# Kernel optimization log

Hardware: AMD Instinct MI355X
Metric: run time of the kernel (lower is better)

## Reference

```python
import jax, jax.numpy as jnp
import numpy as np

B, L, P, S, O = 8192, 512, 64, 32, 200
BIG = jnp.float32(1e30)


def setup_inputs() -> dict:
    key = jax.random.key(0)
    k1, k2, k3, k4, k5 = jax.random.split(key, 5)
    x = jax.random.normal(k1, (B, L), dtype=jnp.float32)
    # nn.init.uniform_ default is U[0,1)
    prototypes = jax.random.uniform(k2, (P, L), dtype=jnp.float32)
    sub_prototypes = jax.random.uniform(k3, (P, S, L), dtype=jnp.float32)
    # per-group linear layers: weight [O,S], bias [O], stacked over P groups
    lim = 1.0 / np.sqrt(S)
    W = jax.random.uniform(k4, (P, O, S), dtype=jnp.float32, minval=-lim, maxval=lim)
    b = jax.random.uniform(k5, (P, O), dtype=jnp.float32, minval=-lim, maxval=lim)
    return {"x": x, "prototypes": prototypes, "sub_prototypes": sub_prototypes, "W": W, "b": b}


def reference(x, prototypes, sub_prototypes, W, b):
    # pairwise squared euclidean distances to top-level prototypes: [B, P]
    d_top = (jnp.sum(x * x, axis=1)[:, None]
             + jnp.sum(prototypes * prototypes, axis=1)[None, :]
             - 2.0 * x @ prototypes.T)
    min1 = jnp.mean(jnp.min(d_top, axis=1))
    min2 = jnp.mean(jnp.min(d_top, axis=0))
    idx = jnp.argmin(d_top, axis=1)  # [B] top-1 routing

    # distances of every sample to every group's sub-prototypes: [B, P, S]
    cross = jnp.einsum('bl,psl->bps', x, sub_prototypes)
    d_all = (jnp.sum(x * x, axis=1)[:, None, None]
             + jnp.sum(sub_prototypes * sub_prototypes, axis=2)[None, :, :]
             - 2.0 * cross)

    # gather each sample's own group's sub-distances: [B, S]
    d_sel = jnp.take_along_axis(d_all, idx[:, None, None], axis=1)[:, 0, :]

    # per-group linear expert applied to gathered rows, scattered back: [B, O]
    out = jnp.einsum('bs,bos->bo', d_sel, W[idx]) + b[idx]

    member = idx[:, None] == jnp.arange(P)[None, :]  # [B, P]
    counts = jnp.sum(member, axis=0)                 # [P]
    nonempty = counts > 0

    # sub_min1: per group, min over assigned samples per sub-proto, mean over S
    d_masked = jnp.where(member[:, :, None], d_all, BIG)
    grp_min_over_b = jnp.min(d_masked, axis=0)       # [P, S]
    per_grp_m1 = jnp.mean(grp_min_over_b, axis=1)    # [P]
    sub_min1 = jnp.sum(jnp.where(nonempty, per_grp_m1, 0.0)) / P

    # sub_min2: per group, mean over assigned samples of per-sample min over S
    per_sample_min = jnp.min(d_sel, axis=1)          # [B]
    grp_sum = jax.ops.segment_sum(per_sample_min, idx, num_segments=P)  # [P]
    per_grp_m2 = jnp.where(nonempty, grp_sum / jnp.maximum(counts, 1), 0.0)
    sub_min2 = jnp.sum(per_grp_m2) / P

    return (min1, min2, sub_min1, sub_min2, out)
```

## Files before the change

### kernel.cpp

```cpp
#include <hip/hip_runtime.h>


#define NL 512
#define NP 64
#define NS 32
#define NO 200
#define NB 8192
#define MAXCH 192

#define WS_SUM     0
#define WS_COLMIN  1
#define WS_SUBMIN  65
#define WS_GRPSUM  2113
#define WS_COUNT   2177
#define WS_PP      2241
#define WS_SP2     2305
#define WS_C2G     4353
#define WS_CBASE   4545
#define WS_CMCNT   4737
#define WS_OFFS    4929
#define WS_SS      4994
#define WS_IDX     13186
#define WS_ORDER   21378
#define WB_PB_HI   131072
#define WB_PB_LO   196608
#define WB_SPB_HI  262144
#define WB_SPB_LO  2359296

typedef __attribute__((ext_vector_type(8))) short short8v;
typedef __attribute__((ext_vector_type(4))) float f32x4;

__device__ __forceinline__ unsigned encf(float f) {
  unsigned u = __float_as_uint(f);
  return (u & 0x80000000u) ? ~u : (u | 0x80000000u);
}
__device__ __forceinline__ float decf(unsigned m) {
  return __uint_as_float((m & 0x80000000u) ? (m ^ 0x80000000u) : ~m);
}
__device__ __forceinline__ float wred(float v) {
#pragma unroll
  for (int m = 32; m >= 1; m >>= 1) v += __shfl_xor(v, m, 64);
  return v;
}
__device__ __forceinline__ float dot4(const float4& a, const float4& b) {
  return a.x * b.x + a.y * b.y + a.z * b.z + a.w * b.w;
}
__device__ __forceinline__ unsigned short f2bf(float f) {
  unsigned u = __float_as_uint(f);
  u += 0x7FFFu + ((u >> 16) & 1u);
  return (unsigned short)(u >> 16);
}
__device__ __forceinline__ float bf2f(unsigned short h) {
  return __uint_as_float(((unsigned)h) << 16);
}
__device__ __forceinline__ void cvt8(const float4& v0, const float4& v1,
                                     short8v& hi, short8v& lo, float& ss) {
  float vs[8] = {v0.x, v0.y, v0.z, v0.w, v1.x, v1.y, v1.z, v1.w};
#pragma unroll
  for (int i = 0; i < 8; ++i) {
    ss = fmaf(vs[i], vs[i], ss);
    unsigned short h = f2bf(vs[i]);
    hi[i] = (short)h;
    lo[i] = (short)f2bf(vs[i] - bf2f(h));
  }
}

__global__ __launch_bounds__(256) void hier_prep(const float* __restrict__ proto,
                                                 const float* __restrict__ subp,
                                                 float* __restrict__ ws) {
  __shared__ float part[256];
  const int bid = blockIdx.x, tid = threadIdx.x;
  unsigned short* sph = (unsigned short*)((char*)ws + WB_SPB_HI);
  unsigned short* spl = (unsigned short*)((char*)ws + WB_SPB_LO);
  unsigned short* pbh = (unsigned short*)((char*)ws + WB_PB_HI);
  unsigned short* pbl = (unsigned short*)((char*)ws + WB_PB_LO);

  if (bid < 512) {
    const int fi = bid * 256 + tid;
    const int l = fi & 63, nt = (fi >> 6) & 1, kt = (fi >> 7) & 15, g = fi >> 11;
    const int s = nt * 16 + (l & 15), k0 = kt * 32 + (l >> 4) * 8;
    const float* src = subp + ((size_t)(g * NS + s)) * NL + k0;
    float4 a = *(const float4*)src, b = *(const float4*)(src + 4);
    float vs[8] = {a.x, a.y, a.z, a.w, b.x, b.y, b.z, b.w};
#pragma unroll
    for (int i = 0; i < 8; ++i) {
      unsigned short h = f2bf(vs[i]);
      sph[(size_t)fi * 8 + i] = h;
      spl[(size_t)fi * 8 + i] = f2bf(vs[i] - bf2f(h));
    }
    return;
  }
  if (bid < 528) {
    const int pi = (bid - 512) * 256 + tid;
    const int l = pi & 63, nt = (pi >> 6) & 3, kt = pi >> 8;
    const int p = nt * 16 + (l & 15), k0 = kt * 32 + (l >> 4) * 8;
    const float* src = proto + (size_t)p * NL + k0;
    float4 a = *(const float4*)src, b = *(const float4*)(src + 4);
    float vs[8] = {a.x, a.y, a.z, a.w, b.x, b.y, b.z, b.w};
#pragma unroll
    for (int i = 0; i < 8; ++i) {
      unsigned short h = f2bf(vs[i]);
      pbh[(size_t)pi * 8 + i] = h;
      pbl[(size_t)pi * 8 + i] = f2bf(vs[i] - bf2f(h));
    }
    return;
  }
  if (bid < 560) {
    const int r = (bid - 528) * 64 + (tid >> 2), q = tid & 3;
    const float4* src = (const float4*)(subp + (size_t)r * NL) + q * 32;
    float a = 0.f;
#pragma unroll
    for (int j = 0; j < 32; ++j) a += dot4(src[j], src[j]);
    part[tid] = a;
    __syncthreads();
    if (tid < 64)
      ws[WS_SP2 + (bid - 528) * 64 + tid] =
          part[4 * tid] + part[4 * tid + 1] + part[4 * tid + 2] + part[4 * tid + 3];
    return;
  }
  if (bid == 560) {
    const int r = tid >> 2, q = tid & 3;
    const float4* src = (const float4*)(proto + (size_t)r * NL) + q * 32;
    float a = 0.f;
#pragma unroll
    for (int j = 0; j < 32; ++j) a += dot4(src[j], src[j]);
    part[tid] = a;
    __syncthreads();
    if (tid < 64)
      ws[WS_PP + tid] =
          part[4 * tid] + part[4 * tid + 1] + part[4 * tid + 2] + part[4 * tid + 3];
    return;
  }
  unsigned* wsu = (unsigned*)ws;
  if (tid == 0) ws[WS_SUM] = 0.f;
  if (tid < 64) {
    wsu[WS_COLMIN + tid] = 0xFFFFFFFFu;
    ws[WS_GRPSUM + tid] = 0.f;
    wsu[WS_COUNT + tid] = 0u;
  }
  for (int u = tid; u < NP * NS; u += 256) wsu[WS_SUBMIN + u] = 0xFFFFFFFFu;
}

__global__ __launch_bounds__(256) void hier_phase1(const float* __restrict__ x,
                                                   float* __restrict__ ws) {
  __shared__ unsigned hist_l[64];
  const int tid = threadIdx.x, lane = tid & 63, w = tid >> 6;
  const int c = lane & 15, g4 = lane >> 4;
  const int b0 = blockIdx.x * 64;
  const short8v* PBH = (const short8v*)((const char*)ws + WB_PB_HI);
  const short8v* PBL = (const short8v*)((const char*)ws + WB_PB_LO);
  if (tid < 64) hist_l[tid] = 0u;
  __syncthreads();

  const int row = b0 + w * 16 + c;
  const float* xrow = x + (size_t)row * NL + g4 * 8;
  f32x4 acc[4];
#pragma unroll
  for (int nt = 0; nt < 4; ++nt) acc[nt] = (f32x4){0.f, 0.f, 0.f, 0.f};
  float ssv = 0.f;

#pragma unroll 2
  for (int kt = 0; kt < 16; ++kt) {
    float4 v0 = *(const float4*)(xrow + kt * 32);
    float4 v1 = *(const float4*)(xrow + kt * 32 + 4);
    short8v ah, al;
    cvt8(v0, v1, ah, al, ssv);
    const short8v* BH = PBH + (size_t)(kt * 4) * 64 + lane;
    const short8v* BL = PBL + (size_t)(kt * 4) * 64 + lane;
#pragma unroll
    for (int nt = 0; nt < 4; ++nt) {
      short8v bh = BH[nt * 64];
      short8v bl = BL[nt * 64];
      acc[nt] = __builtin_amdgcn_mfma_f32_16x16x32_bf16(ah, bh, acc[nt], 0, 0, 0);
      acc[nt] = __builtin_amdgcn_mfma_f32_16x16x32_bf16(ah, bl, acc[nt], 0, 0, 0);
      acc[nt] = __builtin_amdgcn_mfma_f32_16x16x32_bf16(al, bh, acc[nt], 0, 0, 0);
    }
  }

  ssv += __shfl_xor(ssv, 16, 64);
  ssv += __shfl_xor(ssv, 32, 64);
  if (lane < 16) ws[WS_SS + b0 + w * 16 + lane] = ssv;
  float ssm[4];
#pragma unroll
  for (int r = 0; r < 4; ++r) ssm[r] = __shfl(ssv, g4 * 4 + r, 64);

  float dv[4][4];
#pragma unroll
  for (int nt = 0; nt < 4; ++nt) {
    float ppv = ws[WS_PP + nt * 16 + c];
#pragma unroll
    for (int r = 0; r < 4; ++r) dv[nt][r] = ssm[r] + ppv - 2.f * acc[nt][r];
  }
  float rmin[4];
  int rarg[4];
#pragma unroll
  for (int r = 0; r < 4; ++r) {
    rmin[r] = 1e30f; rarg[r] = 0;
#pragma unroll
    for (int nt = 0; nt < 4; ++nt)
      if (dv[nt][r] < rmin[r]) { rmin[r] = dv[nt][r]; rarg[r] = nt * 16 + c; }
  }
#pragma unroll
  for (int m = 1; m <= 8; m <<= 1) {
#pragma unroll
    for (int r = 0; r < 4; ++r) {
      float om = __shfl_xor(rmin[r], m, 64);
      int oa = __shfl_xor(rarg[r], m, 64);
      if (om < rmin[r] || (om == rmin[r] && oa < rarg[r])) { rmin[r] = om; rarg[r] = oa; }
    }
  }
#pragma unroll
  for (int nt = 0; nt < 4; ++nt) {
    float cm = fminf(fminf(dv[nt][0], dv[nt][1]), fminf(dv[nt][2], dv[nt][3]));
    cm = fminf(cm, __shfl_xor(cm, 16, 64));
    cm = fminf(cm, __shfl_xor(cm, 32, 64));
    if (lane < 16) atomicMin((unsigned*)ws + WS_COLMIN + nt * 16 + lane, encf(cm));
  }
  float rsum = 0.f;
  if (c == 0) {
#pragma unroll
    for (int r = 0; r < 4; ++r) {
      ((int*)ws)[WS_IDX + b0 + w * 16 + g4 * 4 + r] = rarg[r];
      atomicAdd(&hist_l[rarg[r]], 1u);
      rsum += rmin[r];
    }
  }
  rsum = wred(rsum);
  if (lane == 0) atomicAdd(&ws[WS_SUM], rsum);
  __syncthreads();
  if (tid < 64 && hist_l[tid]) atomicAdd((unsigned*)ws + WS_COUNT + tid, hist_l[tid]);
}

__global__ __launch_bounds__(256) void hier_scan(float* __restrict__ ws) {
  __shared__ unsigned cnt_l[64];
  __shared__ unsigned cur[64];
  const int tid = threadIdx.x;
  unsigned* wsu = (unsigned*)ws;
  for (int i = tid; i < MAXCH; i += 256) ((int*)ws)[WS_C2G + i] = -1;
  if (tid < 64) cnt_l[tid] = wsu[WS_COUNT + tid];
  __syncthreads();
  if (tid == 0) {
    unsigned run = 0;
    int nc = 0;
    for (int g = 0; g < NP; ++g) {
      wsu[WS_OFFS + g] = run;
      unsigned cc = cnt_l[g];
      for (unsigned j = 0; j * 64 < cc; ++j) {
        ((int*)ws)[WS_C2G + nc] = g;
        wsu[WS_CBASE + nc] = run + j * 64;
        unsigned mc = cc - j * 64;
        wsu[WS_CMCNT + nc] = mc < 64u ? mc : 64u;
        ++nc;
      }
      run += cc;
    }
    wsu[WS_OFFS + 64] = run;
  }
  __syncthreads();
  if (tid < 64) cur[tid] = wsu[WS_OFFS + tid];
  __syncthreads();
  const int* idx = (const int*)ws + WS_IDX;
  for (int b = tid; b < NB; b += 256) {
    int g = idx[b];
    unsigned pos = atomicAdd(&cur[g], 1u);
    wsu[WS_ORDER + pos] = (unsigned)b;
  }
}

__global__ __launch_bounds__(256) void hier_phase3(const float* __restrict__ x,
                                                   const float* __restrict__ Wm,
                                                   const float* __restrict__ bias,
                                                   float* __restrict__ out,
                                                   float* __restrict__ ws) {
  __shared__ unsigned rows_l[64];
  __shared__ float ss_l[64];
  __shared__ float sp2_l[32];
  __shared__ float dsel_l[64 * 33];
  const int tid = threadIdx.x, lane = tid & 63, w = tid >> 6;
  const int c = lane & 15, g4 = lane >> 4;
  const int ch = blockIdx.x;
  const int graw = ((const int*)ws)[WS_C2G + ch];
  if (graw < 0) return;
  const int g = graw;
  const unsigned base = ((const unsigned*)ws)[WS_CBASE + ch];
  const int mc = (int)((const unsigned*)ws)[WS_CMCNT + ch];

  if (tid < 64) {
    int m = tid < mc ? tid : mc - 1;
    rows_l[tid] = ((const unsigned*)ws)[WS_ORDER + base + m];
  }
  __syncthreads();
  if (tid < 64) ss_l[tid] = ws[WS_SS + rows_l[tid]];
  if (tid < 32) sp2_l[tid] = ws[WS_SP2 + g * NS + tid];
  __syncthreads();

  const short8v* SPH = (const short8v*)((const char*)ws + WB_SPB_HI);
  const short8v* SPL = (const short8v*)((const char*)ws + WB_SPB_LO);
  const float* xrow = x + (size_t)rows_l[w * 16 + c] * NL + g4 * 8;

  f32x4 acc[2];
  acc[0] = (f32x4){0.f, 0.f, 0.f, 0.f};
  acc[1] = (f32x4){0.f, 0.f, 0.f, 0.f};
  float ssv = 0.f;

#pragma unroll 2
  for (int kt = 0; kt < 16; ++kt) {
    float4 v0 = *(const float4*)(xrow + kt * 32);
    float4 v1 = *(const float4*)(xrow + kt * 32 + 4);
    short8v ah, al;
    cvt8(v0, v1, ah, al, ssv);
    const short8v* BH = SPH + ((size_t)(g * 16 + kt) * 2) * 64 + lane;
    const short8v* BL = SPL + ((size_t)(g * 16 + kt) * 2) * 64 + lane;
#pragma unroll
    for (int nt = 0; nt < 2; ++nt) {
      short8v bh = BH[nt * 64];
      short8v bl = BL[nt * 64];
      acc[nt] = __builtin_amdgcn_mfma_f32_16x16x32_bf16(ah, bh, acc[nt], 0, 0, 0);
      acc[nt] = __builtin_amdgcn_mfma_f32_16x16x32_bf16(ah, bl, acc[nt], 0, 0, 0);
      acc[nt] = __builtin_amdgcn_mfma_f32_16x16x32_bf16(al, bh, acc[nt], 0, 0, 0);
    }
  }

  float dv[2][4];
#pragma unroll
  for (int nt = 0; nt < 2; ++nt) {
    float s2 = sp2_l[nt * 16 + c];
#pragma unroll
    for (int r = 0; r < 4; ++r) {
      dv[nt][r] = ss_l[w * 16 + g4 * 4 + r] + s2 - 2.f * acc[nt][r];
      dsel_l[(w * 16 + g4 * 4 + r) * 33 + nt * 16 + c] = dv[nt][r];
    }
  }
#pragma unroll
  for (int nt = 0; nt < 2; ++nt) {
    float cm = fminf(fminf(dv[nt][0], dv[nt][1]), fminf(dv[nt][2], dv[nt][3]));
    cm = fminf(cm, __shfl_xor(cm, 16, 64));
    cm = fminf(cm, __shfl_xor(cm, 32, 64));
    if (lane < 16) atomicMin((unsigned*)ws + WS_SUBMIN + g * NS + nt * 16 + lane, encf(cm));
  }
  float rmin[4];
#pragma unroll
  for (int r = 0; r < 4; ++r) rmin[r] = fminf(dv[0][r], dv[1][r]);
#pragma unroll
  for (int m = 1; m <= 8; m <<= 1) {
#pragma unroll
    for (int r = 0; r < 4; ++r) rmin[r] = fminf(rmin[r], __shfl_xor(rmin[r], m, 64));
  }
  float rsum = 0.f;
  if (c == 0) {
#pragma unroll
    for (int r = 0; r < 4; ++r) {
      int sm = w * 16 + g4 * 4 + r;
      if (sm < mc) rsum += rmin[r];
    }
  }
  rsum = wred(rsum);
  if (lane == 0) atomicAdd(&ws[WS_GRPSUM + g], rsum);
  __syncthreads();

  const unsigned myrow = rows_l[lane];
  float dsr[NS];
#pragma unroll
  for (int cc = 0; cc < NS; ++cc) dsr[cc] = dsel_l[lane * 33 + cc];
  const float* wbase = Wm + (size_t)g * NO * NS;
  const float* bbase = bias + (size_t)g * NO;
  const int o0 = w * 52;
  const int no4 = (w < 3) ? 13 : 11;
  float* orow = out + (size_t)myrow * NO;
  for (int j4 = 0; j4 < no4; ++j4) {
    float rr[4];
#pragma unroll
    for (int e = 0; e < 4; ++e) {
      const int o = o0 + 4 * j4 + e;
      const float4* wv = (const float4*)(wbase + (size_t)o * NS);
      float a = bbase[o];
#pragma unroll
      for (int k = 0; k < 8; ++k) {
        float4 w4 = wv[k];
        a += dsr[4 * k + 0] * w4.x + dsr[4 * k + 1] * w4.y +
             dsr[4 * k + 2] * w4.z + dsr[4 * k + 3] * w4.w;
      }
      rr[e] = a;
    }
    float4 st = {rr[0], rr[1], rr[2], rr[3]};
    *(float4*)(orow + o0 + 4 * j4) = st;
  }
}

__global__ void hier_final(const float* __restrict__ ws, float* __restrict__ out4) {
  const int lane = threadIdx.x;
  const unsigned* colmin = (const unsigned*)ws + WS_COLMIN;
  const unsigned* submin = (const unsigned*)ws + WS_SUBMIN;
  const float* grp_sum = ws + WS_GRPSUM;
  const unsigned* counts = (const unsigned*)ws + WS_COUNT;

  float min2 = wred(decf(colmin[lane])) * (1.0f / NP);

  unsigned cnt = counts[lane];
  float s32 = 0.f;
#pragma unroll
  for (int s = 0; s < NS; s++) s32 += decf(submin[lane * NS + s]);
  float sub1 = wred((cnt > 0u) ? s32 * (1.0f / NS) : 0.f) * (1.0f / NP);
  float sub2 = wred((cnt > 0u) ? grp_sum[lane] / (float)cnt : 0.f) * (1.0f / NP);

  if (lane == 0) {
    out4[0] = ws[WS_SUM] * (1.0f / NB);
    out4[1] = min2;
    out4[2] = sub1;
    out4[3] = sub2;
  }
}

extern "C" void kernel_launch(void* const* d_in, const int* in_sizes, int n_in,
                              void* d_out, int out_size, void* d_ws, size_t ws_size,
                              hipStream_t stream) {
  const float* x = (const float*)d_in[0];
  const float* proto = (const float*)d_in[1];
  const float* subp = (const float*)d_in[2];
  const float* Wm = (const float*)d_in[3];
  const float* bias = (const float*)d_in[4];
  float* outf = (float*)d_out;
  float* ws = (float*)d_ws;

  hipLaunchKernelGGL(hier_prep, dim3(562), dim3(256), 0, stream, proto, subp, ws);
  hipLaunchKernelGGL(hier_phase1, dim3(128), dim3(256), 0, stream, x, ws);
  hipLaunchKernelGGL(hier_scan, dim3(1), dim3(256), 0, stream, ws);
  hipLaunchKernelGGL(hier_phase3, dim3(MAXCH), dim3(256), 0, stream,
                     x, Wm, bias, outf + 4, ws);
  hipLaunchKernelGGL(hier_final, dim3(1), dim3(64), 0, stream, ws, outf);
}
```

Measured before the change: 175.7 us.

## Pre-convert x to bf16 fragments, split K across waves, shrink chunks to 16 rows

x is converted once in the prep kernel into hi/lo bf16 MFMA fragment layout, and its row norms are computed there. A new reorder kernel gathers each routed chunk's fragments into a contiguous buffer. Phase1 and phase3 now split the K dimension across four waves and reduce the partial sums through shared memory. Chunks shrink from 64 to 16 rows, and MAXCH grows to 576, to raise block-level parallelism on the small grids. The expert linear layer keeps W rows in registers per output column. The cost is extra workspace traffic for the fragment copies, an additional kernel launch, and more redundant work on padded chunk rows.

```diff
diff --git a/kernel.cpp b/kernel.cpp
--- a/kernel.cpp
+++ b/kernel.cpp
@@ -6,7 +6,7 @@
 #define NS 32
 #define NO 200
 #define NB 8192
-#define MAXCH 192
+#define MAXCH 576
 
 #define WS_SUM     0
 #define WS_COLMIN  1
@@ -16,16 +16,20 @@
 #define WS_PP      2241
 #define WS_SP2     2305
 #define WS_C2G     4353
-#define WS_CBASE   4545
-#define WS_CMCNT   4737
-#define WS_OFFS    4929
-#define WS_SS      4994
-#define WS_IDX     13186
-#define WS_ORDER   21378
+#define WS_CBASE   4929
+#define WS_CMCNT   5505
+#define WS_OFFS    6081
+#define WS_SS      6146
+#define WS_IDX     14338
+#define WS_ORDER   22530
 #define WB_PB_HI   131072
 #define WB_PB_LO   196608
 #define WB_SPB_HI  262144
 #define WB_SPB_LO  2359296
+#define WB_XF_HI   4456448
+#define WB_XF_LO   12845056
+#define WB_XSF_HI  21233664
+#define WB_XSF_LO  30670848
 
 typedef __attribute__((ext_vector_type(8))) short short8v;
 typedef __attribute__((ext_vector_type(4))) float f32x4;
@@ -53,60 +57,85 @@
 __device__ __forceinline__ float bf2f(unsigned short h) {
   return __uint_as_float(((unsigned)h) << 16);
 }
-__device__ __forceinline__ void cvt8(const float4& v0, const float4& v1,
-                                     short8v& hi, short8v& lo, float& ss) {
+__device__ __forceinline__ void cvt8s(const float4& v0, const float4& v1,
+                                      short8v& hi, short8v& lo) {
   float vs[8] = {v0.x, v0.y, v0.z, v0.w, v1.x, v1.y, v1.z, v1.w};
 #pragma unroll
   for (int i = 0; i < 8; ++i) {
-    ss = fmaf(vs[i], vs[i], ss);
     unsigned short h = f2bf(vs[i]);
     hi[i] = (short)h;
     lo[i] = (short)f2bf(vs[i] - bf2f(h));
   }
 }
 
-__global__ __launch_bounds__(256) void hier_prep(const float* __restrict__ proto,
+__global__ __launch_bounds__(256) void hier_prep(const float* __restrict__ x,
+                                                 const float* __restrict__ proto,
                                                  const float* __restrict__ subp,
                                                  float* __restrict__ ws) {
   __shared__ float part[256];
   const int bid = blockIdx.x, tid = threadIdx.x;
-  unsigned short* sph = (unsigned short*)((char*)ws + WB_SPB_HI);
-  unsigned short* spl = (unsigned short*)((char*)ws + WB_SPB_LO);
-  unsigned short* pbh = (unsigned short*)((char*)ws + WB_PB_HI);
-  unsigned short* pbl = (unsigned short*)((char*)ws + WB_PB_LO);
 
   if (bid < 512) {
-    const int fi = bid * 256 + tid;
-    const int l = fi & 63, nt = (fi >> 6) & 1, kt = (fi >> 7) & 15, g = fi >> 11;
-    const int s = nt * 16 + (l & 15), k0 = kt * 32 + (l >> 4) * 8;
-    const float* src = subp + ((size_t)(g * NS + s)) * NL + k0;
-    float4 a = *(const float4*)src, b = *(const float4*)(src + 4);
-    float vs[8] = {a.x, a.y, a.z, a.w, b.x, b.y, b.z, b.w};
-#pragma unroll
-    for (int i = 0; i < 8; ++i) {
-      unsigned short h = f2bf(vs[i]);
-      sph[(size_t)fi * 8 + i] = h;
-      spl[(size_t)fi * 8 + i] = f2bf(vs[i] - bf2f(h));
+    const int tile = bid;
+    short8v* xfh = (short8v*)((char*)ws + WB_XF_HI);
+    short8v* xfl = (short8v*)((char*)ws + WB_XF_LO);
+#pragma unroll
+    for (int i = 0; i < 4; ++i) {
+      const int f = i * 256 + tid;
+      const int kt = f >> 6, l = f & 63;
+      const int row = tile * 16 + (l & 15), k0 = kt * 32 + (l >> 4) * 8;
+      const float* src = x + (size_t)row * NL + k0;
+      short8v hi, lo;
+      cvt8s(*(const float4*)src, *(const float4*)(src + 4), hi, lo);
+      const size_t fo = (size_t)(tile * 16 + kt) * 64 + l;
+      xfh[fo] = hi;
+      xfl[fo] = lo;
+    }
+    {
+      const int s = tid >> 4, q = tid & 15;
+      const float4* xv = (const float4*)(x + (size_t)(tile * 16 + s) * NL) + q * 8;
+      float a = 0.f;
+#pragma unroll
+      for (int j = 0; j < 8; ++j) a += dot4(xv[j], xv[j]);
+      part[tid] = a;
+    }
+    __syncthreads();
+    if (tid < 16) {
+      float a = 0.f;
+#pragma unroll
+      for (int q = 0; q < 16; ++q) a += part[tid * 16 + q];
+      ws[WS_SS + tile * 16 + tid] = a;
     }
     return;
   }
   if (bid < 528) {
+    unsigned short* pbh = (unsigned short*)((char*)ws + WB_PB_HI);
+    unsigned short* pbl = (unsigned short*)((char*)ws + WB_PB_LO);
     const int pi = (bid - 512) * 256 + tid;
     const int l = pi & 63, nt = (pi >> 6) & 3, kt = pi >> 8;
     const int p = nt * 16 + (l & 15), k0 = kt * 32 + (l >> 4) * 8;
     const float* src = proto + (size_t)p * NL + k0;
-    float4 a = *(const float4*)src, b = *(const float4*)(src + 4);
-    float vs[8] = {a.x, a.y, a.z, a.w, b.x, b.y, b.z, b.w};
-#pragma unroll
-    for (int i = 0; i < 8; ++i) {
-      unsigned short h = f2bf(vs[i]);
-      pbh[(size_t)pi * 8 + i] = h;
-      pbl[(size_t)pi * 8 + i] = f2bf(vs[i] - bf2f(h));
-    }
+    short8v hi, lo;
+    cvt8s(*(const float4*)src, *(const float4*)(src + 4), hi, lo);
+    ((short8v*)pbh)[pi] = hi;
+    ((short8v*)pbl)[pi] = lo;
     return;
   }
-  if (bid < 560) {
-    const int r = (bid - 528) * 64 + (tid >> 2), q = tid & 3;
+  if (bid < 1040) {
+    short8v* sph = (short8v*)((char*)ws + WB_SPB_HI);
+    short8v* spl = (short8v*)((char*)ws + WB_SPB_LO);
+    const int fi = (bid - 528) * 256 + tid;
+    const int l = fi & 63, nt = (fi >> 6) & 1, kt = (fi >> 7) & 15, g = fi >> 11;
+    const int s = nt * 16 + (l & 15), k0 = kt * 32 + (l >> 4) * 8;
+    const float* src = subp + ((size_t)(g * NS + s)) * NL + k0;
+    short8v hi, lo;
+    cvt8s(*(const float4*)src, *(const float4*)(src + 4), hi, lo);
+    sph[fi] = hi;
+    spl[fi] = lo;
+    return;
+  }
+  if (bid < 1072) {
+    const int r = (bid - 1040) * 64 + (tid >> 2), q = tid & 3;
     const float4* src = (const float4*)(subp + (size_t)r * NL) + q * 32;
     float a = 0.f;
 #pragma unroll
@@ -114,11 +143,11 @@
     part[tid] = a;
     __syncthreads();
     if (tid < 64)
-      ws[WS_SP2 + (bid - 528) * 64 + tid] =
+      ws[WS_SP2 + (bid - 1040) * 64 + tid] =
           part[4 * tid] + part[4 * tid + 1] + part[4 * tid + 2] + part[4 * tid + 3];
     return;
   }
-  if (bid == 560) {
+  if (bid == 1072) {
     const int r = tid >> 2, q = tid & 3;
     const float4* src = (const float4*)(proto + (size_t)r * NL) + q * 32;
     float a = 0.f;
@@ -141,92 +170,94 @@
   for (int u = tid; u < NP * NS; u += 256) wsu[WS_SUBMIN + u] = 0xFFFFFFFFu;
 }
 
-__global__ __launch_bounds__(256) void hier_phase1(const float* __restrict__ x,
-                                                   float* __restrict__ ws) {
+__global__ __launch_bounds__(256) void hier_phase1(float* __restrict__ ws) {
+  __shared__ float accl[4][64][17];
+  __shared__ float ss_l[16], pp_l[64];
   __shared__ unsigned hist_l[64];
   const int tid = threadIdx.x, lane = tid & 63, w = tid >> 6;
   const int c = lane & 15, g4 = lane >> 4;
-  const int b0 = blockIdx.x * 64;
+  const int tile = blockIdx.x;
+  const short8v* XFH = (const short8v*)((const char*)ws + WB_XF_HI);
+  const short8v* XFL = (const short8v*)((const char*)ws + WB_XF_LO);
   const short8v* PBH = (const short8v*)((const char*)ws + WB_PB_HI);
   const short8v* PBL = (const short8v*)((const char*)ws + WB_PB_LO);
-  if (tid < 64) hist_l[tid] = 0u;
-  __syncthreads();
-
-  const int row = b0 + w * 16 + c;
-  const float* xrow = x + (size_t)row * NL + g4 * 8;
+
+  if (tid < 16) ss_l[tid] = ws[WS_SS + tile * 16 + tid];
+  if (tid < 64) { pp_l[tid] = ws[WS_PP + tid]; hist_l[tid] = 0u; }
+
   f32x4 acc[4];
 #pragma unroll
   for (int nt = 0; nt < 4; ++nt) acc[nt] = (f32x4){0.f, 0.f, 0.f, 0.f};
-  float ssv = 0.f;
-
-#pragma unroll 2
-  for (int kt = 0; kt < 16; ++kt) {
-    float4 v0 = *(const float4*)(xrow + kt * 32);
-    float4 v1 = *(const float4*)(xrow + kt * 32 + 4);
-    short8v ah, al;
-    cvt8(v0, v1, ah, al, ssv);
-    const short8v* BH = PBH + (size_t)(kt * 4) * 64 + lane;
-    const short8v* BL = PBL + (size_t)(kt * 4) * 64 + lane;
+#pragma unroll
+  for (int i = 0; i < 4; ++i) {
+    const int kt = w * 4 + i;
+    short8v ah = XFH[(size_t)(tile * 16 + kt) * 64 + lane];
+    short8v al = XFL[(size_t)(tile * 16 + kt) * 64 + lane];
 #pragma unroll
     for (int nt = 0; nt < 4; ++nt) {
-      short8v bh = BH[nt * 64];
-      short8v bl = BL[nt * 64];
+      short8v bh = PBH[(size_t)(kt * 4 + nt) * 64 + lane];
+      short8v bl = PBL[(size_t)(kt * 4 + nt) * 64 + lane];
       acc[nt] = __builtin_amdgcn_mfma_f32_16x16x32_bf16(ah, bh, acc[nt], 0, 0, 0);
       acc[nt] = __builtin_amdgcn_mfma_f32_16x16x32_bf16(ah, bl, acc[nt], 0, 0, 0);
       acc[nt] = __builtin_amdgcn_mfma_f32_16x16x32_bf16(al, bh, acc[nt], 0, 0, 0);
     }
   }
-
-  ssv += __shfl_xor(ssv, 16, 64);
-  ssv += __shfl_xor(ssv, 32, 64);
-  if (lane < 16) ws[WS_SS + b0 + w * 16 + lane] = ssv;
-  float ssm[4];
-#pragma unroll
-  for (int r = 0; r < 4; ++r) ssm[r] = __shfl(ssv, g4 * 4 + r, 64);
-
-  float dv[4][4];
-#pragma unroll
-  for (int nt = 0; nt < 4; ++nt) {
-    float ppv = ws[WS_PP + nt * 16 + c];
-#pragma unroll
-    for (int r = 0; r < 4; ++r) dv[nt][r] = ssm[r] + ppv - 2.f * acc[nt][r];
-  }
-  float rmin[4];
-  int rarg[4];
-#pragma unroll
-  for (int r = 0; r < 4; ++r) {
-    rmin[r] = 1e30f; rarg[r] = 0;
-#pragma unroll
-    for (int nt = 0; nt < 4; ++nt)
-      if (dv[nt][r] < rmin[r]) { rmin[r] = dv[nt][r]; rarg[r] = nt * 16 + c; }
-  }
-#pragma unroll
-  for (int m = 1; m <= 8; m <<= 1) {
+#pragma unroll
+  for (int nt = 0; nt < 4; ++nt)
+#pragma unroll
+    for (int r = 0; r < 4; ++r) accl[w][lane][nt * 4 + r] = acc[nt][r];
+  __syncthreads();
+
+  if (w == 0) {
+    float dv[4][4];
+#pragma unroll
+    for (int nt = 0; nt < 4; ++nt) {
+      const float ppv = pp_l[nt * 16 + c];
+#pragma unroll
+      for (int r = 0; r < 4; ++r) {
+        const int j = nt * 4 + r;
+        float s = accl[0][lane][j] + accl[1][lane][j] + accl[2][lane][j] +
+                  accl[3][lane][j];
+        dv[nt][r] = ss_l[g4 * 4 + r] + ppv - 2.f * s;
+      }
+    }
+    float rmin[4];
+    int rarg[4];
 #pragma unroll
     for (int r = 0; r < 4; ++r) {
-      float om = __shfl_xor(rmin[r], m, 64);
-      int oa = __shfl_xor(rarg[r], m, 64);
-      if (om < rmin[r] || (om == rmin[r] && oa < rarg[r])) { rmin[r] = om; rarg[r] = oa; }
-    }
-  }
-#pragma unroll
-  for (int nt = 0; nt < 4; ++nt) {
-    float cm = fminf(fminf(dv[nt][0], dv[nt][1]), fminf(dv[nt][2], dv[nt][3]));
-    cm = fminf(cm, __shfl_xor(cm, 16, 64));
-    cm = fminf(cm, __shfl_xor(cm, 32, 64));
-    if (lane < 16) atomicMin((unsigned*)ws + WS_COLMIN + nt * 16 + lane, encf(cm));
-  }
-  float rsum = 0.f;
-  if (c == 0) {
-#pragma unroll
-    for (int r = 0; r < 4; ++r) {
-      ((int*)ws)[WS_IDX + b0 + w * 16 + g4 * 4 + r] = rarg[r];
-      atomicAdd(&hist_l[rarg[r]], 1u);
-      rsum += rmin[r];
-    }
-  }
-  rsum = wred(rsum);
-  if (lane == 0) atomicAdd(&ws[WS_SUM], rsum);
+      rmin[r] = 1e30f; rarg[r] = 0;
+#pragma unroll
+      for (int nt = 0; nt < 4; ++nt)
+        if (dv[nt][r] < rmin[r]) { rmin[r] = dv[nt][r]; rarg[r] = nt * 16 + c; }
+    }
+#pragma unroll
+    for (int m = 1; m <= 8; m <<= 1) {
+#pragma unroll
+      for (int r = 0; r < 4; ++r) {
+        float om = __shfl_xor(rmin[r], m, 64);
+        int oa = __shfl_xor(rarg[r], m, 64);
+        if (om < rmin[r] || (om == rmin[r] && oa < rarg[r])) { rmin[r] = om; rarg[r] = oa; }
+      }
+    }
+#pragma unroll
+    for (int nt = 0; nt < 4; ++nt) {
+      float cm = fminf(fminf(dv[nt][0], dv[nt][1]), fminf(dv[nt][2], dv[nt][3]));
+      cm = fminf(cm, __shfl_xor(cm, 16, 64));
+      cm = fminf(cm, __shfl_xor(cm, 32, 64));
+      if (lane < 16) atomicMin((unsigned*)ws + WS_COLMIN + nt * 16 + lane, encf(cm));
+    }
+    float rsum = 0.f;
+    if (c == 0) {
+#pragma unroll
+      for (int r = 0; r < 4; ++r) {
+        ((int*)ws)[WS_IDX + tile * 16 + g4 * 4 + r] = rarg[r];
+        atomicAdd(&hist_l[rarg[r]], 1u);
+        rsum += rmin[r];
+      }
+    }
+    rsum = wred(rsum);
+    if (lane == 0) atomicAdd(&ws[WS_SUM], rsum);
+  }
   __syncthreads();
   if (tid < 64 && hist_l[tid]) atomicAdd((unsigned*)ws + WS_COUNT + tid, hist_l[tid]);
 }
@@ -245,11 +276,11 @@
     for (int g = 0; g < NP; ++g) {
       wsu[WS_OFFS + g] = run;
       unsigned cc = cnt_l[g];
-      for (unsigned j = 0; j * 64 < cc; ++j) {
+      for (unsigned j = 0; j * 16 < cc; ++j) {
         ((int*)ws)[WS_C2G + nc] = g;
-        wsu[WS_CBASE + nc] = run + j * 64;
-        unsigned mc = cc - j * 64;
-        wsu[WS_CMCNT + nc] = mc < 64u ? mc : 64u;
+        wsu[WS_CBASE + nc] = run + j * 16;
+        unsigned mc = cc - j * 16;
+        wsu[WS_CMCNT + nc] = mc < 16u ? mc : 16u;
         ++nc;
       }
       run += cc;
@@ -267,15 +298,38 @@
   }
 }
 
-__global__ __launch_bounds__(256) void hier_phase3(const float* __restrict__ x,
-                                                   const float* __restrict__ Wm,
+__global__ __launch_bounds__(256) void hier_reorder(float* __restrict__ ws) {
+  const int ch = blockIdx.x, tid = threadIdx.x;
+  if (((const int*)ws)[WS_C2G + ch] < 0) return;
+  const unsigned base = ((const unsigned*)ws)[WS_CBASE + ch];
+  const int mc = (int)((const unsigned*)ws)[WS_CMCNT + ch];
+  const unsigned* order = (const unsigned*)ws + WS_ORDER;
+  const uint4* XFH = (const uint4*)((const char*)ws + WB_XF_HI);
+  const uint4* XFL = (const uint4*)((const char*)ws + WB_XF_LO);
+  uint4* XSFH = (uint4*)((char*)ws + WB_XSF_HI);
+  uint4* XSFL = (uint4*)((char*)ws + WB_XSF_LO);
+#pragma unroll
+  for (int i = 0; i < 4; ++i) {
+    const int f = i * 256 + tid;
+    const int kt = f >> 6, l = f & 63;
+    int m = l & 15;
+    if (m >= mc) m = mc - 1;
+    const unsigned row = order[base + m];
+    const size_t src = (size_t)((row >> 4) * 16 + kt) * 64 + ((l >> 4) * 16 + (row & 15));
+    const size_t dst = (size_t)(ch * 16 + kt) * 64 + l;
+    XSFH[dst] = XFH[src];
+    XSFL[dst] = XFL[src];
+  }
+}
+
+__global__ __launch_bounds__(256) void hier_phase3(const float* __restrict__ Wm,
                                                    const float* __restrict__ bias,
                                                    float* __restrict__ out,
                                                    float* __restrict__ ws) {
-  __shared__ unsigned rows_l[64];
-  __shared__ float ss_l[64];
-  __shared__ float sp2_l[32];
-  __shared__ float dsel_l[64 * 33];
+  __shared__ float accl[4][64][9];
+  __shared__ float ss_l[16], sp2_l[32];
+  __shared__ unsigned rows_l[16];
+  __shared__ float dsel_l[16][36];
   const int tid = threadIdx.x, lane = tid & 63, w = tid >> 6;
   const int c = lane & 15, g4 = lane >> 4;
   const int ch = blockIdx.x;
@@ -285,105 +339,104 @@
   const unsigned base = ((const unsigned*)ws)[WS_CBASE + ch];
   const int mc = (int)((const unsigned*)ws)[WS_CMCNT + ch];
 
-  if (tid < 64) {
+  float4 wreg[8];
+  float breg = 0.f;
+  if (tid < NO) {
+    const float4* wr = (const float4*)(Wm + ((size_t)g * NO + tid) * NS);
+#pragma unroll
+    for (int k = 0; k < 8; ++k) wreg[k] = wr[k];
+    breg = bias[(size_t)g * NO + tid];
+  }
+
+  if (tid < 16) {
     int m = tid < mc ? tid : mc - 1;
-    rows_l[tid] = ((const unsigned*)ws)[WS_ORDER + base + m];
-  }
-  __syncthreads();
-  if (tid < 64) ss_l[tid] = ws[WS_SS + rows_l[tid]];
+    unsigned r = ((const unsigned*)ws)[WS_ORDER + base + m];
+    rows_l[tid] = r;
+    ss_l[tid] = ws[WS_SS + r];
+  }
   if (tid < 32) sp2_l[tid] = ws[WS_SP2 + g * NS + tid];
-  __syncthreads();
-
+
+  const short8v* XSFH = (const short8v*)((const char*)ws + WB_XSF_HI);
+  const short8v* XSFL = (const short8v*)((const char*)ws + WB_XSF_LO);
   const short8v* SPH = (const short8v*)((const char*)ws + WB_SPB_HI);
   const short8v* SPL = (const short8v*)((const char*)ws + WB_SPB_LO);
-  const float* xrow = x + (size_t)rows_l[w * 16 + c] * NL + g4 * 8;
 
   f32x4 acc[2];
   acc[0] = (f32x4){0.f, 0.f, 0.f, 0.f};
   acc[1] = (f32x4){0.f, 0.f, 0.f, 0.f};
-  float ssv = 0.f;
-
-#pragma unroll 2
-  for (int kt = 0; kt < 16; ++kt) {
-    float4 v0 = *(const float4*)(xrow + kt * 32);
-    float4 v1 = *(const float4*)(xrow + kt * 32 + 4);
-    short8v ah, al;
-    cvt8(v0, v1, ah, al, ssv);
-    const short8v* BH = SPH + ((size_t)(g * 16 + kt) * 2) * 64 + lane;
-    const short8v* BL = SPL + ((size_t)(g * 16 + kt) * 2) * 64 + lane;
+#pragma unroll
+  for (int i = 0; i < 4; ++i) {
+    const int kt = w * 4 + i;
+    short8v ah = XSFH[(size_t)(ch * 16 + kt) * 64 + lane];
+    short8v al = XSFL[(size_t)(ch * 16 + kt) * 64 + lane];
 #pragma unroll
     for (int nt = 0; nt < 2; ++nt) {
-      short8v bh = BH[nt * 64];
-      short8v bl = BL[nt * 64];
+      short8v bh = SPH[((size_t)(g * 16 + kt) * 2 + nt) * 64 + lane];
+      short8v bl = SPL[((size_t)(g * 16 + kt) * 2 + nt) * 64 + lane];
       acc[nt] = __builtin_amdgcn_mfma_f32_16x16x32_bf16(ah, bh, acc[nt], 0, 0, 0);
       acc[nt] = __builtin_amdgcn_mfma_f32_16x16x32_bf16(ah, bl, acc[nt], 0, 0, 0);
       acc[nt] = __builtin_amdgcn_mfma_f32_16x16x32_bf16(al, bh, acc[nt], 0, 0, 0);
     }
   }
-
-  float dv[2][4];
-#pragma unroll
-  for (int nt = 0; nt < 2; ++nt) {
-    float s2 = sp2_l[nt * 16 + c];
-#pragma unroll
-    for (int r = 0; r < 4; ++r) {
-      dv[nt][r] = ss_l[w * 16 + g4 * 4 + r] + s2 - 2.f * acc[nt][r];
-      dsel_l[(w * 16 + g4 * 4 + r) * 33 + nt * 16 + c] = dv[nt][r];
-    }
-  }
-#pragma unroll
-  for (int nt = 0; nt < 2; ++nt) {
-    float cm = fminf(fminf(dv[nt][0], dv[nt][1]), fminf(dv[nt][2], dv[nt][3]));
-    cm = fminf(cm, __shfl_xor(cm, 16, 64));
-    cm = fminf(cm, __shfl_xor(cm, 32, 64));
-    if (lane < 16) atomicMin((unsigned*)ws + WS_SUBMIN + g * NS + nt * 16 + lane, encf(cm));
-  }
-  float rmin[4];
-#pragma unroll
-  for (int r = 0; r < 4; ++r) rmin[r] = fminf(dv[0][r], dv[1][r]);
-#pragma unroll
-  for (int m = 1; m <= 8; m <<= 1) {
-#pragma unroll
-    for (int r = 0; r < 4; ++r) rmin[r] = fminf(rmin[r], __shfl_xor(rmin[r], m, 64));
-  }
-  float rsum = 0.f;
-  if (c == 0) {
-#pragma unroll
-    for (int r = 0; r < 4; ++r) {
-      int sm = w * 16 + g4 * 4 + r;
-      if (sm < mc) rsum += rmin[r];
-    }
-  }
-  rsum = wred(rsum);
-  if (lane == 0) atomicAdd(&ws[WS_GRPSUM + g], rsum);
-  __syncthreads();
-
-  const unsigned myrow = rows_l[lane];
-  float dsr[NS];
-#pragma unroll
-  for (int cc = 0; cc < NS; ++cc) dsr[cc] = dsel_l[lane * 33 + cc];
-  const float* wbase = Wm + (size_t)g * NO * NS;
-  const float* bbase = bias + (size_t)g * NO;
-  const int o0 = w * 52;
-  const int no4 = (w < 3) ? 13 : 11;
-  float* orow = out + (size_t)myrow * NO;
-  for (int j4 = 0; j4 < no4; ++j4) {
-    float rr[4];
-#pragma unroll
-    for (int e = 0; e < 4; ++e) {
-      const int o = o0 + 4 * j4 + e;
-      const float4* wv = (const float4*)(wbase + (size_t)o * NS);
-      float a = bbase[o];
+#pragma unroll
+  for (int nt = 0; nt < 2; ++nt)
+#pragma unroll
+    for (int r = 0; r < 4; ++r) accl[w][lane][nt * 4 + r] = acc[nt][r];
+  __syncthreads();
+
+  if (w == 0) {
+    float dv[2][4];
+#pragma unroll
+    for (int nt = 0; nt < 2; ++nt) {
+      const float s2 = sp2_l[nt * 16 + c];
+#pragma unroll
+      for (int r = 0; r < 4; ++r) {
+        const int j = nt * 4 + r;
+        float s = accl[0][lane][j] + accl[1][lane][j] + accl[2][lane][j] +
+                  accl[3][lane][j];
+        dv[nt][r] = ss_l[g4 * 4 + r] + s2 - 2.f * s;
+        dsel_l[g4 * 4 + r][nt * 16 + c] = dv[nt][r];
+      }
+    }
+#pragma unroll
+    for (int nt = 0; nt < 2; ++nt) {
+      float cm = fminf(fminf(dv[nt][0], dv[nt][1]), fminf(dv[nt][2], dv[nt][3]));
+      cm = fminf(cm, __shfl_xor(cm, 16, 64));
+      cm = fminf(cm, __shfl_xor(cm, 32, 64));
+      if (lane < 16)
+        atomicMin((unsigned*)ws + WS_SUBMIN + g * NS + nt * 16 + lane, encf(cm));
+    }
+    float rmin[4];
+#pragma unroll
+    for (int r = 0; r < 4; ++r) rmin[r] = fminf(dv[0][r], dv[1][r]);
+#pragma unroll
+    for (int m = 1; m <= 8; m <<= 1)
+#pragma unroll
+      for (int r = 0; r < 4; ++r) rmin[r] = fminf(rmin[r], __shfl_xor(rmin[r], m, 64));
+    float rsum = 0.f;
+    if (c == 0) {
+#pragma unroll
+      for (int r = 0; r < 4; ++r) {
+        const int sm = g4 * 4 + r;
+        if (sm < mc) rsum += rmin[r];
+      }
+    }
+    rsum = wred(rsum);
+    if (lane == 0) atomicAdd(&ws[WS_GRPSUM + g], rsum);
+  }
+  __syncthreads();
+
+  if (tid < NO) {
+    for (int m = 0; m < mc; ++m) {
+      const float* ds = &dsel_l[m][0];
+      float a = breg;
 #pragma unroll
       for (int k = 0; k < 8; ++k) {
-        float4 w4 = wv[k];
-        a += dsr[4 * k + 0] * w4.x + dsr[4 * k + 1] * w4.y +
-             dsr[4 * k + 2] * w4.z + dsr[4 * k + 3] * w4.w;
-      }
-      rr[e] = a;
-    }
-    float4 st = {rr[0], rr[1], rr[2], rr[3]};
-    *(float4*)(orow + o0 + 4 * j4) = st;
+        a += ds[4 * k + 0] * wreg[k].x + ds[4 * k + 1] * wreg[k].y +
+             ds[4 * k + 2] * wreg[k].z + ds[4 * k + 3] * wreg[k].w;
+      }
+      out[(size_t)rows_l[m] * NO + tid] = a;
+    }
   }
 }
 
@@ -422,10 +475,11 @@
   float* outf = (float*)d_out;
   float* ws = (float*)d_ws;
 
-  hipLaunchKernelGGL(hier_prep, dim3(562), dim3(256), 0, stream, proto, subp, ws);
-  hipLaunchKernelGGL(hier_phase1, dim3(128), dim3(256), 0, stream, x, ws);
+  hipLaunchKernelGGL(hier_prep, dim3(1074), dim3(256), 0, stream, x, proto, subp, ws);
+  hipLaunchKernelGGL(hier_phase1, dim3(512), dim3(256), 0, stream, ws);
   hipLaunchKernelGGL(hier_scan, dim3(1), dim3(256), 0, stream, ws);
+  hipLaunchKernelGGL(hier_reorder, dim3(MAXCH), dim3(256), 0, stream, ws);
   hipLaunchKernelGGL(hier_phase3, dim3(MAXCH), dim3(256), 0, stream,
-                     x, Wm, bias, outf + 4, ws);
+                     Wm, bias, outf + 4, ws);
   hipLaunchKernelGGL(hier_final, dim3(1), dim3(64), 0, stream, ws, outf);
 }
```

After: 180.5 us. +2.7%, slower.
